# Performance work log

Hardware: AMD Instinct MI355X
Metric: run time of the kernel (lower is better)

The kernel has to match this reference:

```python
import jax, jax.numpy as jnp
import numpy as np

T, B, I, H = 512, 32, 512, 512

def setup_inputs() -> dict:
    key = jax.random.key(0)
    k1, k2, k3 = jax.random.split(key, 3)
    x = jax.random.normal(k1, (T, B, I), dtype=jnp.float32)
    h0 = jnp.zeros((B, H), dtype=jnp.float32)
    W_ih = jax.random.normal(k2, (3 * H, I), dtype=jnp.float32) * (1.0 / np.sqrt(H))
    # diagonal recurrent weights, one vector per gate (r, z, n), uniform(-1, 1)
    w_hh = jax.random.uniform(k3, (3, H), dtype=jnp.float32, minval=-1.0, maxval=1.0)
    return {"x": x, "h0": h0, "W_ih": W_ih, "w_hh": w_hh}

def reference(x, h0, W_ih, w_hh):
    # Precompute input-side gate pre-activations for all timesteps: (T, B, 3H)
    gx = jnp.einsum('tbi,gi->tbg', x, W_ih)
    xr, xz, xn = jnp.split(gx, 3, axis=-1)  # each (T, B, H)
    w_r, w_z, w_n = w_hh[0], w_hh[1], w_hh[2]  # each (H,)

    def step(h, g):
        gr, gz, gn = g
        r = jax.nn.sigmoid(gr + w_r * h)
        z = jax.nn.sigmoid(gz + w_z * h)
        n = jnp.tanh(gn + r * (w_n * h))
        h_new = (1.0 - z) * n + z * h
        return h_new, h_new

    h_last, out = jax.lax.scan(step, h0, (xr, xz, xn))
    # out: (T, B, H) all hidden states; h_last: (1, B, H) final state (GRU convention)
    return out, h_last[None, :, :]
```

## Files before the change

kernel.cpp:

```cpp
#include <hip/hip_runtime.h>
#include <hip/hip_bf16.h>
#include <stdint.h>

#define T_DIM 512
#define B_DIM 32
#define K_DIM 512
#define H_DIM 512
#define N_DIM 1536
#define M_DIM 16384

typedef __bf16 bf16_t;
typedef bf16_t bf16x8 __attribute__((ext_vector_type(8)));
typedef float floatx4 __attribute__((ext_vector_type(4)));

#define LOG2E 1.442695041f
#define TWO_LOG2E 2.885390082f

__device__ __forceinline__ unsigned int f2bf_bits(float f) {
  uint32_t u = __builtin_bit_cast(uint32_t, f);
  u += 0x7FFFu + ((u >> 16) & 1u);
  return u >> 16;
}

__global__ void convert_both_kernel(const float* __restrict__ x,
                                    unsigned short* __restrict__ xb,
                                    const float* __restrict__ W,
                                    unsigned short* __restrict__ Wb) {
  int bid = blockIdx.x;
  const float* src;
  unsigned short* dst;
  int i;
  if (bid < 4096) {
    i = (bid * 256 + threadIdx.x) * 8;
    src = x + i;
    dst = xb + i;
  } else {
    i = ((bid - 4096) * 256 + threadIdx.x) * 8;
    int n = i >> 9;
    int k = i & 511;
    int p6 = n / 6;
    int sub = n - p6 * 6;
    int hodd = (sub >= 3) ? 1 : 0;
    int g = sub - hodd * 3;
    int h = p6 * 2 + hodd;
    src = W + ((g << 9) + h) * 512 + k;
    dst = Wb + i;
  }
  const float4* p = (const float4*)src;
  float4 f0 = p[0];
  float4 f1 = p[1];
  uint4 v;
  v.x = f2bf_bits(f0.x) | (f2bf_bits(f0.y) << 16);
  v.y = f2bf_bits(f0.z) | (f2bf_bits(f0.w) << 16);
  v.z = f2bf_bits(f1.x) | (f2bf_bits(f1.y) << 16);
  v.w = f2bf_bits(f1.z) | (f2bf_bits(f1.w) << 16);
  *(uint4*)dst = v;
}

__global__ __launch_bounds__(256) void gemm_bf16_kernel(
    const unsigned short* __restrict__ A, const unsigned short* __restrict__ Bm,
    _Float16* __restrict__ C) {
  __shared__ bf16_t smem[16384];
  const int tid = threadIdx.x;
  const int lane = tid & 63;
  const int w = tid >> 6;
  const int tileM = blockIdx.x * 128;
  const int tileN = blockIdx.y * 128;
  const int waveM = w & 1;
  const int waveN = w >> 1;
  const int lm = lane & 15;
  const int lg = lane >> 4;

  floatx4 acc[4][4] = {};

  for (int k0 = 0; k0 < K_DIM; k0 += 64) {
#pragma unroll
    for (int j = 0; j < 4; ++j) {
      int s = j * 256 + tid;
      int row = s >> 3;
      int cpos = s & 7;
      int kc = cpos ^ (row & 7);
      bf16_t* la = smem + (j * 256 + w * 64) * 8;
      const unsigned short* ga = A + (size_t)(tileM + row) * K_DIM + k0 + kc * 8;
      __builtin_amdgcn_global_load_lds(
          (const __attribute__((address_space(1))) unsigned int*)ga,
          (__attribute__((address_space(3))) unsigned int*)la, 16, 0, 0);
      bf16_t* lb = smem + 8192 + (j * 256 + w * 64) * 8;
      const unsigned short* gb = Bm + (size_t)(tileN + row) * K_DIM + k0 + kc * 8;
      __builtin_amdgcn_global_load_lds(
          (const __attribute__((address_space(1))) unsigned int*)gb,
          (__attribute__((address_space(3))) unsigned int*)lb, 16, 0, 0);
    }
    __syncthreads();

#pragma unroll
    for (int ks = 0; ks < 2; ++ks) {
      bf16x8 af[4], bfg[4];
#pragma unroll
      for (int i = 0; i < 4; ++i) {
        int row = waveM * 64 + i * 16 + lm;
        int c = ks * 4 + lg;
        af[i] = *(const bf16x8*)(smem + row * 64 + (c ^ (row & 7)) * 8);
      }
#pragma unroll
      for (int j = 0; j < 4; ++j) {
        int row = waveN * 64 + j * 16 + lm;
        int c = ks * 4 + lg;
        bfg[j] = *(const bf16x8*)(smem + 8192 + row * 64 + (c ^ (row & 7)) * 8);
      }
#pragma unroll
      for (int i = 0; i < 4; ++i)
#pragma unroll
        for (int j = 0; j < 4; ++j)
          acc[i][j] = __builtin_amdgcn_mfma_f32_16x16x32_bf16(af[i], bfg[j],
                                                              acc[i][j], 0, 0, 0);
    }
    __syncthreads();
  }

  _Float16* ep = (_Float16*)smem + w * 4096;
#pragma unroll
  for (int j = 0; j < 4; ++j) {
    const int cl = lm + j * 16;
    const int sub = (tileN + waveN * 64 + cl) % 6;
    const float scl = (sub == 2 || sub == 5) ? TWO_LOG2E : -LOG2E;
#pragma unroll
    for (int i = 0; i < 4; ++i)
#pragma unroll
      for (int r = 0; r < 4; ++r) {
        int rl = (lane >> 4) * 4 + r + 16 * i;
        ep[rl * 64 + cl] = (_Float16)(scl * acc[i][j][r]);
      }
  }
  const int q = lm;
  const int rgrp = lane >> 4;
  const size_t crow0 = (size_t)(tileM + waveM * 64);
  const int ccol = tileN + waveN * 64 + q * 4;
#pragma unroll
  for (int k = 0; k < 16; ++k) {
    int rl = rgrp + 4 * k;
    uint2 v = *(const uint2*)(ep + rl * 64 + q * 4);
    *(uint2*)(C + (crow0 + rl) * N_DIM + ccol) = v;
  }
}

__global__ __launch_bounds__(64) void indgru_scan_kernel(
    const _Float16* __restrict__ gx, const float* __restrict__ h0,
    const float* __restrict__ w_hh, float* __restrict__ out,
    float* __restrict__ hlast) {
  const int idx = blockIdx.x * 64 + threadIdx.x;
  const int b = idx >> 9;
  const int h = idx & (H_DIM - 1);
  const float wr = -LOG2E * w_hh[h];
  const float wz = -LOG2E * w_hh[H_DIM + h];
  const float wn = TWO_LOG2E * w_hh[2 * H_DIM + h];
  const int sh = (h & 1) << 4;
  float hv = h0[idx];

  const char* base = (const char*)(gx + (size_t)b * N_DIM + (h >> 1) * 6) + ((h & 1) << 2);
  float* outp = out + (size_t)b * H_DIM + h;

  constexpr int D = 16;
  constexpr size_t TSTRIDE = (size_t)B_DIM * N_DIM * sizeof(_Float16);
  uint2 pq[D];
#pragma unroll
  for (int t = 0; t < D; ++t)
    pq[t] = *(const uint2*)(base + (size_t)t * TSTRIDE);

  auto cvt16 = [](uint32_t bits) {
    return (float)__builtin_bit_cast(_Float16, (unsigned short)bits);
  };

  for (int t0 = 0; t0 < T_DIM - D; t0 += D) {
#pragma unroll
    for (int s = 0; s < D; ++s) {
      const int t = t0 + s;
      uint2 q = pq[s];
      pq[s] = *(const uint2*)(base + (size_t)(t + D) * TSTRIDE);
      asm volatile("" ::: "memory");
      uint64_t v = (((uint64_t)q.y << 32) | q.x) >> sh;
      float gr = cvt16((uint32_t)v);
      float gz = cvt16((uint32_t)(v >> 16));
      float gn = cvt16((uint32_t)(v >> 32));
      float ar = fmaf(wr, hv, gr);
      float az = fmaf(wz, hv, gz);
      float t1 = wn * hv;
      float er = __builtin_amdgcn_exp2f(ar);
      float ez = __builtin_amdgcn_exp2f(az);
      float r = __builtin_amdgcn_rcpf(1.0f + er);
      float z = __builtin_amdgcn_rcpf(1.0f + ez);
      float en = __builtin_amdgcn_exp2f(fmaf(r, t1, gn));
      float u = __builtin_amdgcn_rcpf(1.0f + en);
      float n = fmaf(-2.0f, u, 1.0f);
      float zh = z * hv;
      float omz = 1.0f - z;
      hv = fmaf(n, omz, zh);
      outp[(size_t)t * (B_DIM * H_DIM)] = hv;
    }
  }
#pragma unroll
  for (int s = 0; s < D; ++s) {
    const int t = T_DIM - D + s;
    uint2 q = pq[s];
    uint64_t v = (((uint64_t)q.y << 32) | q.x) >> sh;
    float gr = cvt16((uint32_t)v);
    float gz = cvt16((uint32_t)(v >> 16));
    float gn = cvt16((uint32_t)(v >> 32));
    float ar = fmaf(wr, hv, gr);
    float az = fmaf(wz, hv, gz);
    float t1 = wn * hv;
    float er = __builtin_amdgcn_exp2f(ar);
    float ez = __builtin_amdgcn_exp2f(az);
    float r = __builtin_amdgcn_rcpf(1.0f + er);
    float z = __builtin_amdgcn_rcpf(1.0f + ez);
    float en = __builtin_amdgcn_exp2f(fmaf(r, t1, gn));
    float u = __builtin_amdgcn_rcpf(1.0f + en);
    float n = fmaf(-2.0f, u, 1.0f);
    float zh = z * hv;
    float omz = 1.0f - z;
    hv = fmaf(n, omz, zh);
    outp[(size_t)t * (B_DIM * H_DIM)] = hv;
  }
  hlast[idx] = hv;
}

extern "C" void kernel_launch(void* const* d_in, const int* in_sizes, int n_in,
                              void* d_out, int out_size, void* d_ws, size_t ws_size,
                              hipStream_t stream) {
  const float* x    = (const float*)d_in[0];
  const float* h0   = (const float*)d_in[1];
  const float* W_ih = (const float*)d_in[2];
  const float* w_hh = (const float*)d_in[3];

  float* out = (float*)d_out;
  float* hlast = out + (size_t)T_DIM * B_DIM * H_DIM;

  char* ws = (char*)d_ws;
  unsigned short* xb = (unsigned short*)ws;
  unsigned short* Wb = (unsigned short*)(ws + 16777216);
  _Float16* gx = (_Float16*)(ws + 16777216 + 1572864);

  convert_both_kernel<<<4480, 256, 0, stream>>>(x, xb, W_ih, Wb);

  dim3 grid(M_DIM / 128, N_DIM / 128);
  gemm_bf16_kernel<<<grid, 256, 0, stream>>>(xb, Wb, gx);

  indgru_scan_kernel<<<256, 64, 0, stream>>>(gx, h0, w_hh, out, hlast);
}
```

Measured before the change: 160.7 us.

## Enlarge GEMM tile to 256x128 with 8 waves and deepen scan prefetch

The GEMM block grows from 128x128 with 4 waves to 256x128 with 8 waves, so each B tile loaded into LDS is reused across twice as many rows. The epilogue is restaged in two halves to fit the smaller per-wave LDS scratch. The scan kernel's register prefetch depth doubles from 16 to 32 timesteps to hide more gx load latency. The cost is fewer GEMM blocks (768 vs 1536), more LDS per block and higher register pressure in the scan.

After: 149.7 us. 1.07x faster.

```diff
diff --git a/kernel.cpp b/kernel.cpp
--- a/kernel.cpp
+++ b/kernel.cpp
@@ -57,17 +57,17 @@
   *(uint4*)dst = v;
 }
 
-__global__ __launch_bounds__(256) void gemm_bf16_kernel(
+__global__ __launch_bounds__(512, 4) void gemm_bf16_kernel(
     const unsigned short* __restrict__ A, const unsigned short* __restrict__ Bm,
     _Float16* __restrict__ C) {
-  __shared__ bf16_t smem[16384];
+  __shared__ bf16_t smem[24576];
   const int tid = threadIdx.x;
   const int lane = tid & 63;
   const int w = tid >> 6;
-  const int tileM = blockIdx.x * 128;
+  const int tileM = blockIdx.x * 256;
   const int tileN = blockIdx.y * 128;
-  const int waveM = w & 1;
-  const int waveN = w >> 1;
+  const int waveM = w & 3;
+  const int waveN = w >> 2;
   const int lm = lane & 15;
   const int lg = lane >> 4;
 
@@ -75,17 +75,22 @@
 
   for (int k0 = 0; k0 < K_DIM; k0 += 64) {
 #pragma unroll
-    for (int j = 0; j < 4; ++j) {
-      int s = j * 256 + tid;
+    for (int g = 0; g < 4; ++g) {
+      int s = g * 512 + tid;
       int row = s >> 3;
-      int cpos = s & 7;
-      int kc = cpos ^ (row & 7);
-      bf16_t* la = smem + (j * 256 + w * 64) * 8;
+      int kc = (s & 7) ^ (row & 7);
+      bf16_t* la = smem + (g * 512 + w * 64) * 8;
       const unsigned short* ga = A + (size_t)(tileM + row) * K_DIM + k0 + kc * 8;
       __builtin_amdgcn_global_load_lds(
           (const __attribute__((address_space(1))) unsigned int*)ga,
           (__attribute__((address_space(3))) unsigned int*)la, 16, 0, 0);
-      bf16_t* lb = smem + 8192 + (j * 256 + w * 64) * 8;
+    }
+#pragma unroll
+    for (int g = 0; g < 2; ++g) {
+      int s = g * 512 + tid;
+      int row = s >> 3;
+      int kc = (s & 7) ^ (row & 7);
+      bf16_t* lb = smem + 16384 + (g * 512 + w * 64) * 8;
       const unsigned short* gb = Bm + (size_t)(tileN + row) * K_DIM + k0 + kc * 8;
       __builtin_amdgcn_global_load_lds(
           (const __attribute__((address_space(1))) unsigned int*)gb,
@@ -106,7 +111,7 @@
       for (int j = 0; j < 4; ++j) {
         int row = waveN * 64 + j * 16 + lm;
         int c = ks * 4 + lg;
-        bfg[j] = *(const bf16x8*)(smem + 8192 + row * 64 + (c ^ (row & 7)) * 8);
+        bfg[j] = *(const bf16x8*)(smem + 16384 + row * 64 + (c ^ (row & 7)) * 8);
       }
 #pragma unroll
       for (int i = 0; i < 4; ++i)
@@ -118,29 +123,34 @@
     __syncthreads();
   }
 
-  _Float16* ep = (_Float16*)smem + w * 4096;
-#pragma unroll
-  for (int j = 0; j < 4; ++j) {
-    const int cl = lm + j * 16;
-    const int sub = (tileN + waveN * 64 + cl) % 6;
-    const float scl = (sub == 2 || sub == 5) ? TWO_LOG2E : -LOG2E;
-#pragma unroll
-    for (int i = 0; i < 4; ++i)
-#pragma unroll
-      for (int r = 0; r < 4; ++r) {
-        int rl = (lane >> 4) * 4 + r + 16 * i;
-        ep[rl * 64 + cl] = (_Float16)(scl * acc[i][j][r]);
-      }
-  }
+  _Float16* ep = (_Float16*)smem + w * 2048;
   const int q = lm;
   const int rgrp = lane >> 4;
   const size_t crow0 = (size_t)(tileM + waveM * 64);
   const int ccol = tileN + waveN * 64 + q * 4;
 #pragma unroll
-  for (int k = 0; k < 16; ++k) {
-    int rl = rgrp + 4 * k;
-    uint2 v = *(const uint2*)(ep + rl * 64 + q * 4);
-    *(uint2*)(C + (crow0 + rl) * N_DIM + ccol) = v;
+  for (int p = 0; p < 2; ++p) {
+#pragma unroll
+    for (int il = 0; il < 2; ++il) {
+      const int i = 2 * p + il;
+#pragma unroll
+      for (int j = 0; j < 4; ++j) {
+        const int cl = lm + j * 16;
+        const int sub = (tileN + waveN * 64 + cl) % 6;
+        const float scl = (sub == 2 || sub == 5) ? TWO_LOG2E : -LOG2E;
+#pragma unroll
+        for (int r = 0; r < 4; ++r) {
+          int rl = (lane >> 4) * 4 + r + 16 * il;
+          ep[rl * 64 + cl] = (_Float16)(scl * acc[i][j][r]);
+        }
+      }
+    }
+#pragma unroll
+    for (int k = 0; k < 8; ++k) {
+      int rl = rgrp + 4 * k;
+      uint2 v = *(const uint2*)(ep + rl * 64 + q * 4);
+      *(uint2*)(C + (crow0 + p * 32 + rl) * N_DIM + ccol) = v;
+    }
   }
 }
 
@@ -160,7 +170,7 @@
   const char* base = (const char*)(gx + (size_t)b * N_DIM + (h >> 1) * 6) + ((h & 1) << 2);
   float* outp = out + (size_t)b * H_DIM + h;
 
-  constexpr int D = 16;
+  constexpr int D = 32;
   constexpr size_t TSTRIDE = (size_t)B_DIM * N_DIM * sizeof(_Float16);
   uint2 pq[D];
 #pragma unroll
@@ -242,8 +252,8 @@
 
   convert_both_kernel<<<4480, 256, 0, stream>>>(x, xb, W_ih, Wb);
 
-  dim3 grid(M_DIM / 128, N_DIM / 128);
-  gemm_bf16_kernel<<<grid, 256, 0, stream>>>(xb, Wb, gx);
+  dim3 grid(M_DIM / 256, N_DIM / 128);
+  gemm_bf16_kernel<<<grid, 512, 0, stream>>>(xb, Wb, gx);
 
   indgru_scan_kernel<<<256, 64, 0, stream>>>(gx, h0, w_hh, out, hlast);
 }
```
